# Kernel optimization log

Measured on AMD Instinct MI355X. Metric: run time of the kernel, lower is better.

The kernel has to match this reference:

```python
import math
import jax, jax.numpy as jnp
import numpy as np

EMBED_DIM = 1024
NUM_HEADS = 16
HEAD_DIM = EMBED_DIM // NUM_HEADS


def setup_inputs() -> dict:
    key = jax.random.key(0)
    ks = jax.random.split(key, 10)
    B, S, E = 2, 2048, EMBED_DIM
    x = jax.random.normal(ks[0], (B, S, E), dtype=jnp.float32)
    mask = jax.random.randint(ks[1], (B, S), 0, 2, dtype=jnp.int32)
    s = 1.0 / math.sqrt(E)
    Wq = jax.random.normal(ks[2], (E, E), dtype=jnp.float32) * s
    bq = jnp.zeros((E,), dtype=jnp.float32)
    Wk = jax.random.normal(ks[3], (E, E), dtype=jnp.float32) * s
    bk = jnp.zeros((E,), dtype=jnp.float32)
    Wv = jax.random.normal(ks[4], (E, E), dtype=jnp.float32) * s
    bv = jnp.zeros((E,), dtype=jnp.float32)
    Wo = jax.random.normal(ks[5], (E, E), dtype=jnp.float32) * s
    bo = jnp.zeros((E,), dtype=jnp.float32)
    return {"x": x, "mask": mask, "Wq": Wq, "bq": bq, "Wk": Wk, "bk": bk,
            "Wv": Wv, "bv": bv, "Wo": Wo, "bo": bo}


def reference(x, mask, Wq, bq, Wk, bk, Wv, bv, Wo, bo):
    B, S, E = x.shape
    H, D = NUM_HEADS, HEAD_DIM
    scale = math.sqrt(D)  # ScaledDotProductAttention built with head_dim

    def split_heads(t):
        return t.reshape(B, S, H, D).transpose(0, 2, 1, 3)  # [B,H,S,D]

    q = split_heads(x @ Wq + bq)
    k = split_heads(x @ Wk + bk)
    v = split_heads(x @ Wv + bv)

    scores = jnp.einsum('bhqd,bhkd->bhqk', q, k) / scale  # [B,H,S,S]
    m = mask[:, None, None, :].astype(scores.dtype)        # [B,1,1,S]
    neg = jnp.finfo(scores.dtype).min
    scores = jnp.where(m == 0, neg, scores)
    aw = jax.nn.softmax(scores, axis=-1)
    # post-softmax mask renormalization (as in the torch module)
    aw = aw * m
    denom = aw.sum(axis=-1, keepdims=True)
    aw = jnp.where(denom > 0, aw / jnp.where(denom > 0, denom, 1.0), 0.0)

    ctx = jnp.einsum('bhqk,bhkd->bhqd', aw, v)             # [B,H,S,D]
    ctx = ctx.transpose(0, 2, 1, 3).reshape(B, S, E)
    out = ctx @ Wo + bo
    return out
```

## Files before the change

### kernel.cpp

```cpp
#include <hip/hip_runtime.h>

typedef _Float16 half8 __attribute__((ext_vector_type(8)));
typedef _Float16 half4v __attribute__((ext_vector_type(4)));
typedef _Float16 h2 __attribute__((ext_vector_type(2)));
typedef float f4 __attribute__((ext_vector_type(4)));

#define ASYNC_COPY16(ldsp, gp)                                                     \
  __builtin_amdgcn_global_load_lds((__attribute__((address_space(1))) void*)(gp),  \
                                   (__attribute__((address_space(3))) void*)(ldsp),\
                                   16, 0, 0)

__device__ __forceinline__ f4 mfma16(half8 a, half8 b, f4 c) {
  return __builtin_amdgcn_mfma_f32_16x16x32_f16(a, b, c, 0, 0, 0);
}

__device__ __forceinline__ h2 pack2(float a, float b) {
  return __builtin_bit_cast(h2, __builtin_amdgcn_cvt_pkrtz(a, b));
}

#if defined(__has_builtin)
#if __has_builtin(__builtin_amdgcn_exp2f)
#define EXP2(x) __builtin_amdgcn_exp2f(x)
#endif
#endif
#ifndef EXP2
#define EXP2(x) __expf((x) * 0.69314718056f)
#endif
#define KSCALE 0.18033688011f
#define FIXMAX 10.0f


__global__ __launch_bounds__(256) void k_prep(
    const float* __restrict__ x, _Float16* __restrict__ xh,
    const float* __restrict__ Wq, const float* __restrict__ Wk,
    const float* __restrict__ Wv, const float* __restrict__ Wo,
    _Float16* __restrict__ wqkvT, _Float16* __restrict__ woT) {
  __shared__ float tw[32][33];
  const int bid = blockIdx.x, t = threadIdx.x;
  if (bid < 4096) {
    int i = (bid * 256 + t) * 4;
    f4 v = *(const f4*)(x + i);
    half4v h;
    h[0] = (_Float16)v[0]; h[1] = (_Float16)v[1];
    h[2] = (_Float16)v[2]; h[3] = (_Float16)v[3];
    *(half4v*)(xh + i) = h;
    return;
  }
  const int idx = bid - 4096;
  const int z = idx >> 10, rem = idx & 1023;
  const int n0 = (rem & 31) * 32, k0 = (rem >> 5) * 32;
  const float* w = (z == 0) ? Wq : (z == 1) ? Wk : (z == 2) ? Wv : Wo;
  _Float16* wt = (z == 3) ? woT : wqkvT + (size_t)z * 1048576;
  const int tx = t & 31, ty = t >> 5;
  for (int j = 0; j < 32; j += 8) tw[ty + j][tx] = w[(size_t)(k0 + ty + j) * 1024 + n0 + tx];
  __syncthreads();
  for (int j = 0; j < 32; j += 8)
    wt[(size_t)(n0 + ty + j) * 1024 + k0 + tx] = (_Float16)tw[tx][ty + j];
}

__global__ __launch_bounds__(256) void k_gemm_proj(
    const _Float16* __restrict__ A, const _Float16* __restrict__ Bt,
    const float* __restrict__ bq, const float* __restrict__ bk, const float* __restrict__ bv,
    _Float16* __restrict__ Qo, _Float16* __restrict__ Ko, _Float16* __restrict__ Vto) {
  __shared__ __align__(16) _Float16 As[128 * 32];
  __shared__ __align__(16) _Float16 Bs[128 * 32];
  const int t = threadIdx.x, lane = t & 63, w = t >> 6;
  const int qd = lane >> 4, lr = lane & 15;
  const int m0 = blockIdx.y * 128, n0 = blockIdx.x * 128;
  const int wm = (w & 1) * 64, wn = (w >> 1) * 64;
  const f4 z4 = {0.f, 0.f, 0.f, 0.f};
  f4 acc[4][4];
#pragma unroll
  for (int i = 0; i < 4; ++i)
#pragma unroll
    for (int j = 0; j < 4; ++j) acc[i][j] = z4;

  const int c0 = t, c1 = t + 256;
  for (int k0 = 0; k0 < 1024; k0 += 32) {
    const _Float16* ga0 = A + (size_t)(m0 + (c0 >> 2)) * 1024 + k0 + (c0 & 3) * 8;
    const _Float16* ga1 = A + (size_t)(m0 + (c1 >> 2)) * 1024 + k0 + (c1 & 3) * 8;
    const _Float16* gb0 = Bt + (size_t)(n0 + (c0 >> 2)) * 1024 + k0 + (c0 & 3) * 8;
    const _Float16* gb1 = Bt + (size_t)(n0 + (c1 >> 2)) * 1024 + k0 + (c1 & 3) * 8;
    char* la = (char*)As + w * 1024;
    char* lb = (char*)Bs + w * 1024;
    ASYNC_COPY16(la, ga0);
    ASYNC_COPY16(la + 4096, ga1);
    ASYNC_COPY16(lb, gb0);
    ASYNC_COPY16(lb + 4096, gb1);
    __syncthreads();
    half8 af[4], bf[4];
#pragma unroll
    for (int i = 0; i < 4; ++i)
      af[i] = *(const half8*)(As + (wm + i * 16 + lr) * 32 + qd * 8);
#pragma unroll
    for (int j = 0; j < 4; ++j)
      bf[j] = *(const half8*)(Bs + (wn + j * 16 + lr) * 32 + qd * 8);
#pragma unroll
    for (int i = 0; i < 4; ++i)
#pragma unroll
      for (int j = 0; j < 4; ++j) acc[i][j] = mfma16(af[i], bf[j], acc[i][j]);
    __syncthreads();
  }

  const int mat = n0 >> 10;
  const float* bias = (mat == 0) ? bq : (mat == 1) ? bk : bv;
  if (mat == 2) {
#pragma unroll
    for (int i = 0; i < 4; ++i)
#pragma unroll
      for (int j = 0; j < 4; ++j) {
        int n = (n0 + wn + j * 16 + lr) & 1023;
        int hh = n >> 6, d = n & 63;
        int mb = m0 + wm + i * 16 + qd * 4;
        int bb = mb >> 11, sb = mb & 2047;
        float bval = bias[n];
        half4v hv;
#pragma unroll
        for (int r = 0; r < 4; ++r) hv[r] = (_Float16)(acc[i][j][r] + bval);
        *(half4v*)(Vto + ((size_t)(bb * 16 + hh) * 64 + d) * 2048 + sb) = hv;
      }
  } else {
    _Float16* outp = (mat == 0) ? Qo : Ko;
    const float scl = (mat == 0) ? KSCALE : 1.f;
#pragma unroll
    for (int i = 0; i < 4; ++i)
#pragma unroll
      for (int j = 0; j < 4; ++j)
#pragma unroll
        for (int r = 0; r < 4; ++r) {
          int m = m0 + wm + i * 16 + qd * 4 + r;
          int n = (n0 + wn + j * 16 + lr) & 1023;
          float v = (acc[i][j][r] + bias[n]) * scl;
          int bb = m >> 11, s = m & 2047, hh = n >> 6, d = n & 63;
          outp[(size_t)((bb * 16 + hh) * 2048 + s) * 64 + d] = (_Float16)v;
        }
  }
}

__global__ __launch_bounds__(256, 2) void k_attn(
    const _Float16* __restrict__ Qg, const _Float16* __restrict__ Kg,
    const _Float16* __restrict__ Vtg, const int* __restrict__ maskg,
    _Float16* __restrict__ Op, float* __restrict__ ml) {
  __shared__ __align__(16) _Float16 Ks[64][72];
  __shared__ __align__(16) _Float16 Vts[64][72];
  __shared__ __align__(16) _Float16 Pq[4][16][72];
  __shared__ float Msk[64];

  const int bh = blockIdx.y;
  const int b = bh >> 4;
  const int q0 = blockIdx.x * 256;
  const int z = blockIdx.z;
  const int kb = z * 1024;
  const int t = threadIdx.x, lane = t & 63, w = t >> 6;
  const int qd = lane >> 4, lr = lane & 15;

  half8 qf[4][2];
#pragma unroll
  for (int rt = 0; rt < 4; ++rt)
#pragma unroll
    for (int ks = 0; ks < 2; ++ks)
      qf[rt][ks] = *(const half8*)(Qg + (size_t)(bh * 2048 + q0 + w * 64 + rt * 16 + lr) * 64 +
                                   ks * 32 + qd * 8);

  const f4 z4 = {0.f, 0.f, 0.f, 0.f};
  f4 O[4][4];
  f4 Ol[4];
#pragma unroll
  for (int rt = 0; rt < 4; ++rt) {
    Ol[rt] = z4;
#pragma unroll
    for (int dt = 0; dt < 4; ++dt) O[rt][dt] = z4;
  }
  half8 ones8;
#pragma unroll
  for (int j = 0; j < 8; ++j) ones8[j] = (_Float16)1.f;

  const int sr0 = t >> 3, scc = (t & 7) * 8;
  const int sr1 = sr0 + 32;
  const _Float16* Kbase = Kg + (size_t)bh * 2048 * 64 + (size_t)kb * 64;
  const _Float16* Vtbase = Vtg + (size_t)bh * 64 * 2048 + kb;

  f4 kr0 = *(const f4*)(Kbase + (size_t)sr0 * 64 + scc);
  f4 kr1 = *(const f4*)(Kbase + (size_t)sr1 * 64 + scc);
  f4 vr0 = *(const f4*)(Vtbase + (size_t)sr0 * 2048 + scc);
  f4 vr1 = *(const f4*)(Vtbase + (size_t)sr1 * 2048 + scc);
  float mval = 0.f;
  if (t < 64) mval = maskg[b * 2048 + kb + t] ? -FIXMAX : -30010.f;

  for (int it = 0; it < 16; ++it) {
    __syncthreads();
    *(f4*)&Ks[sr0][scc] = kr0;
    *(f4*)&Ks[sr1][scc] = kr1;
    *(f4*)&Vts[sr0][scc] = vr0;
    *(f4*)&Vts[sr1][scc] = vr1;
    if (t < 64) Msk[t] = mval;
    __syncthreads();

    if (it < 15) {
      int kk = (it + 1) * 64;
      kr0 = *(const f4*)(Kbase + (size_t)(kk + sr0) * 64 + scc);
      kr1 = *(const f4*)(Kbase + (size_t)(kk + sr1) * 64 + scc);
      vr0 = *(const f4*)(Vtbase + (size_t)sr0 * 2048 + kk + scc);
      vr1 = *(const f4*)(Vtbase + (size_t)sr1 * 2048 + kk + scc);
      if (t < 64) mval = maskg[b * 2048 + kb + kk + t] ? -FIXMAX : -30010.f;
    }

    half8 kf0[4], kf1[4];
#pragma unroll
    for (int kt = 0; kt < 4; ++kt) {
      kf0[kt] = *(const half8*)&Ks[kt * 16 + lr][qd * 8];
      kf1[kt] = *(const half8*)&Ks[kt * 16 + lr][32 + qd * 8];
    }

    half8 bp[4][2];
#pragma unroll
    for (int rtp = 0; rtp < 2; ++rtp) {
      const int r0 = rtp * 2, r1 = rtp * 2 + 1;
      f4 sc[2][4];
#pragma unroll
      for (int kt = 0; kt < 4; ++kt) {
        f4 mv = *(const f4*)&Msk[kt * 16 + qd * 4];
        sc[0][kt] = mv;
        sc[1][kt] = mv;
      }
      __builtin_amdgcn_s_setprio(1);
#pragma unroll
      for (int kt = 0; kt < 4; ++kt) {
        sc[0][kt] = mfma16(kf0[kt], qf[r0][0], sc[0][kt]);
        sc[0][kt] = mfma16(kf1[kt], qf[r0][1], sc[0][kt]);
        sc[1][kt] = mfma16(kf0[kt], qf[r1][0], sc[1][kt]);
        sc[1][kt] = mfma16(kf1[kt], qf[r1][1], sc[1][kt]);
      }
      __builtin_amdgcn_s_setprio(0);

#pragma unroll
      for (int rr = 0; rr < 2; ++rr) {
        const int rt = rtp * 2 + rr;
#pragma unroll
        for (int kt = 0; kt < 4; ++kt) {
          float p0 = EXP2(sc[rr][kt][0]);
          float p1 = EXP2(sc[rr][kt][1]);
          float p2 = EXP2(sc[rr][kt][2]);
          float p3 = EXP2(sc[rr][kt][3]);
          half4v hv;
          hv.lo = pack2(p0, p1);
          hv.hi = pack2(p2, p3);
          *(half4v*)&Pq[w][lr][kt * 16 + qd * 4] = hv;
        }
        bp[rt][0] = *(const half8*)&Pq[w][lr][qd * 8];
        bp[rt][1] = *(const half8*)&Pq[w][lr][32 + qd * 8];
      }
    }

    __builtin_amdgcn_s_setprio(1);
#pragma unroll
    for (int dt = 0; dt < 4; ++dt) {
      half8 va0 = *(const half8*)&Vts[dt * 16 + lr][qd * 8];
      half8 va1 = *(const half8*)&Vts[dt * 16 + lr][32 + qd * 8];
#pragma unroll
      for (int rt = 0; rt < 4; ++rt) {
        O[rt][dt] = mfma16(va0, bp[rt][0], O[rt][dt]);
        O[rt][dt] = mfma16(va1, bp[rt][1], O[rt][dt]);
      }
    }
#pragma unroll
    for (int rt = 0; rt < 4; ++rt) {
      Ol[rt] = mfma16(ones8, bp[rt][0], Ol[rt]);
      Ol[rt] = mfma16(ones8, bp[rt][1], Ol[rt]);
    }
    __builtin_amdgcn_s_setprio(0);
  }

#pragma unroll
  for (int rt = 0; rt < 4; ++rt) {
    int qrow = q0 + w * 64 + rt * 16 + lr;
    size_t rowi = (size_t)(z * 32 + bh) * 2048 + qrow;
    _Float16* op = Op + rowi * 64;
#pragma unroll
    for (int dt = 0; dt < 4; ++dt) {
      half4v hv;
#pragma unroll
      for (int r = 0; r < 4; ++r) hv[r] = (_Float16)O[rt][dt][r];
      *(half4v*)(op + dt * 16 + qd * 4) = hv;
    }
    if (qd == 0) ml[rowi] = Ol[rt][0];
  }
}

__global__ __launch_bounds__(256) void k_gemm_out(
    const _Float16* __restrict__ Op, const float* __restrict__ ml,
    const _Float16* __restrict__ Bt,
    const float* __restrict__ bo, float* __restrict__ out) {
  __shared__ __align__(16) _Float16 As[64 * 32];
  __shared__ __align__(16) _Float16 Bs[128 * 32];
  const int t = threadIdx.x, lane = t & 63, w = t >> 6;
  const int qd = lane >> 4, lr = lane & 15;
  const int m0 = blockIdx.y * 64, n0 = blockIdx.x * 128;
  const int wm = (w & 1) * 32, wn = (w >> 1) * 64;
  const f4 z4 = {0.f, 0.f, 0.f, 0.f};
  f4 acc[2][4];
#pragma unroll
  for (int i = 0; i < 2; ++i)
#pragma unroll
    for (int j = 0; j < 4; ++j) acc[i][j] = z4;

  const int ar = t >> 2, ac8 = (t & 3) * 8;
  const int m = m0 + ar;
  const int b = m >> 11, s = m & 2047;

  const int c0 = t, c1 = t + 256;
  for (int k0 = 0; k0 < 1024; k0 += 32) {
    const int h = k0 >> 6;
    const int d0 = (k0 & 63) + ac8;
    const size_t r1 = (size_t)(b * 16 + h) * 2048 + s;
    const size_t r2 = r1 + (size_t)32 * 2048;
    const float inv = 1.f / fmaxf(ml[r1] + ml[r2], 1e-20f);
    half8 o1 = *(const half8*)(Op + r1 * 64 + d0);
    half8 o2 = *(const half8*)(Op + r2 * 64 + d0);
    half8 ha;
#pragma unroll
    for (int j = 0; j < 8; ++j)
      ha[j] = (_Float16)(((float)o1[j] + (float)o2[j]) * inv);
    *(half8*)(As + ar * 32 + ac8) = ha;

    const _Float16* gb0 = Bt + (size_t)(n0 + (c0 >> 2)) * 1024 + k0 + (c0 & 3) * 8;
    const _Float16* gb1 = Bt + (size_t)(n0 + (c1 >> 2)) * 1024 + k0 + (c1 & 3) * 8;
    char* lb = (char*)Bs + w * 1024;
    ASYNC_COPY16(lb, gb0);
    ASYNC_COPY16(lb + 4096, gb1);
    __syncthreads();
    half8 af[2], bf[4];
#pragma unroll
    for (int i = 0; i < 2; ++i)
      af[i] = *(const half8*)(As + (wm + i * 16 + lr) * 32 + qd * 8);
#pragma unroll
    for (int j = 0; j < 4; ++j)
      bf[j] = *(const half8*)(Bs + (wn + j * 16 + lr) * 32 + qd * 8);
#pragma unroll
    for (int i = 0; i < 2; ++i)
#pragma unroll
      for (int j = 0; j < 4; ++j) acc[i][j] = mfma16(af[i], bf[j], acc[i][j]);
    __syncthreads();
  }
#pragma unroll
  for (int i = 0; i < 2; ++i)
#pragma unroll
    for (int j = 0; j < 4; ++j)
#pragma unroll
      for (int r = 0; r < 4; ++r) {
        int mm = m0 + wm + i * 16 + qd * 4 + r;
        int n = n0 + wn + j * 16 + lr;
        out[(size_t)mm * 1024 + n] = acc[i][j][r] + bo[n];
      }
}

extern "C" void kernel_launch(void* const* d_in, const int* in_sizes, int n_in,
                              void* d_out, int out_size, void* d_ws, size_t ws_size,
                              hipStream_t stream) {
  const float* x = (const float*)d_in[0];
  const int* mask = (const int*)d_in[1];
  const float* Wq = (const float*)d_in[2];
  const float* bq = (const float*)d_in[3];
  const float* Wk = (const float*)d_in[4];
  const float* bk = (const float*)d_in[5];
  const float* Wv = (const float*)d_in[6];
  const float* bv = (const float*)d_in[7];
  const float* Wo = (const float*)d_in[8];
  const float* bo = (const float*)d_in[9];
  float* out = (float*)d_out;
  char* ws = (char*)d_ws;
  const size_t MB = 1 << 20;

  _Float16* Oph   = (_Float16*)(ws + 0);
  _Float16* xh    = (_Float16*)(ws + 0);
  _Float16* wqkvT = (_Float16*)(ws + 8 * MB);
  _Float16* woT   = (_Float16*)(ws + 16 * MB);
  _Float16* Qh    = (_Float16*)(ws + 18 * MB);
  _Float16* Kh    = (_Float16*)(ws + 26 * MB);
  _Float16* Vth   = (_Float16*)(ws + 34 * MB);
  float*    mlw   = (float*)   (ws + 42 * MB);

  k_prep<<<dim3(8192), dim3(256), 0, stream>>>(x, xh, Wq, Wk, Wv, Wo, wqkvT, woT);
  k_gemm_proj<<<dim3(24, 32), dim3(256), 0, stream>>>(xh, wqkvT, bq, bk, bv, Qh, Kh, Vth);
  k_attn<<<dim3(8, 32, 2), dim3(256), 0, stream>>>(Qh, Kh, Vth, mask, Oph, mlw);
  k_gemm_out<<<dim3(8, 64), dim3(256), 0, stream>>>(Oph, mlw, woT, bo, out);
}
```

Before: 201.2 us.

## Keep softmax probabilities in registers via 16x16x16 MFMA; prefetch combine inputs

The attention kernel no longer writes the exponentiated P tile to shared memory and reads it back in the B-operand layout. It keeps each 16x16 P block in registers and feeds it straight to 16x16x16 f16 MFMAs, matching V reads to that layout. This removes LDS traffic and round-trip latency but doubles the PV MFMA instruction count, each doing half the K-depth. The output projection kernel now precomputes the per-head inverse normalizers once and software-prefetches the next split-K partial outputs across the loop's barrier.

```diff
diff --git a/kernel.cpp b/kernel.cpp
--- a/kernel.cpp
+++ b/kernel.cpp
@@ -12,6 +12,10 @@
 
 __device__ __forceinline__ f4 mfma16(half8 a, half8 b, f4 c) {
   return __builtin_amdgcn_mfma_f32_16x16x32_f16(a, b, c, 0, 0, 0);
+}
+
+__device__ __forceinline__ f4 mfma16x16(half4v a, half4v b, f4 c) {
+  return __builtin_amdgcn_mfma_f32_16x16x16f16(a, b, c, 0, 0, 0);
 }
 
 __device__ __forceinline__ h2 pack2(float a, float b) {
@@ -143,7 +147,6 @@
     _Float16* __restrict__ Op, float* __restrict__ ml) {
   __shared__ __align__(16) _Float16 Ks[64][72];
   __shared__ __align__(16) _Float16 Vts[64][72];
-  __shared__ __align__(16) _Float16 Pq[4][16][72];
   __shared__ float Msk[64];
 
   const int bh = blockIdx.y;
@@ -171,9 +174,9 @@
 #pragma unroll
     for (int dt = 0; dt < 4; ++dt) O[rt][dt] = z4;
   }
-  half8 ones8;
-#pragma unroll
-  for (int j = 0; j < 8; ++j) ones8[j] = (_Float16)1.f;
+  half4v ones4;
+#pragma unroll
+  for (int j = 0; j < 4; ++j) ones4[j] = (_Float16)1.f;
 
   const int sr0 = t >> 3, scc = (t & 7) * 8;
   const int sr1 = sr0 + 32;
@@ -212,7 +215,7 @@
       kf1[kt] = *(const half8*)&Ks[kt * 16 + lr][32 + qd * 8];
     }
 
-    half8 bp[4][2];
+    half4v pf[4][4];
 #pragma unroll
     for (int rtp = 0; rtp < 2; ++rtp) {
       const int r0 = rtp * 2, r1 = rtp * 2 + 1;
@@ -245,29 +248,29 @@
           half4v hv;
           hv.lo = pack2(p0, p1);
           hv.hi = pack2(p2, p3);
-          *(half4v*)&Pq[w][lr][kt * 16 + qd * 4] = hv;
+          pf[rt][kt] = hv;
         }
-        bp[rt][0] = *(const half8*)&Pq[w][lr][qd * 8];
-        bp[rt][1] = *(const half8*)&Pq[w][lr][32 + qd * 8];
       }
     }
 
     __builtin_amdgcn_s_setprio(1);
 #pragma unroll
     for (int dt = 0; dt < 4; ++dt) {
-      half8 va0 = *(const half8*)&Vts[dt * 16 + lr][qd * 8];
-      half8 va1 = *(const half8*)&Vts[dt * 16 + lr][32 + qd * 8];
-#pragma unroll
-      for (int rt = 0; rt < 4; ++rt) {
-        O[rt][dt] = mfma16(va0, bp[rt][0], O[rt][dt]);
-        O[rt][dt] = mfma16(va1, bp[rt][1], O[rt][dt]);
-      }
-    }
-#pragma unroll
-    for (int rt = 0; rt < 4; ++rt) {
-      Ol[rt] = mfma16(ones8, bp[rt][0], Ol[rt]);
-      Ol[rt] = mfma16(ones8, bp[rt][1], Ol[rt]);
-    }
+      half4v va[4];
+#pragma unroll
+      for (int kt = 0; kt < 4; ++kt)
+        va[kt] = *(const half4v*)&Vts[dt * 16 + lr][kt * 16 + qd * 4];
+#pragma unroll
+      for (int rt = 0; rt < 4; ++rt)
+#pragma unroll
+        for (int kt = 0; kt < 4; ++kt)
+          O[rt][dt] = mfma16x16(va[kt], pf[rt][kt], O[rt][dt]);
+    }
+#pragma unroll
+    for (int rt = 0; rt < 4; ++rt)
+#pragma unroll
+      for (int kt = 0; kt < 4; ++kt)
+        Ol[rt] = mfma16x16(ones4, pf[rt][kt], Ol[rt]);
     __builtin_amdgcn_s_setprio(0);
   }
 
@@ -308,15 +311,20 @@
   const int m = m0 + ar;
   const int b = m >> 11, s = m & 2047;
 
+  float invh[16];
+#pragma unroll
+  for (int h = 0; h < 16; ++h) {
+    size_t r1 = (size_t)(b * 16 + h) * 2048 + s;
+    invh[h] = 1.f / fmaxf(ml[r1] + ml[r1 + (size_t)32 * 2048], 1e-20f);
+  }
+
   const int c0 = t, c1 = t + 256;
+  size_t rr1 = (size_t)(b * 16 + 0) * 2048 + s;
+  half8 o1 = *(const half8*)(Op + rr1 * 64 + ac8);
+  half8 o2 = *(const half8*)(Op + (rr1 + (size_t)32 * 2048) * 64 + ac8);
+
   for (int k0 = 0; k0 < 1024; k0 += 32) {
-    const int h = k0 >> 6;
-    const int d0 = (k0 & 63) + ac8;
-    const size_t r1 = (size_t)(b * 16 + h) * 2048 + s;
-    const size_t r2 = r1 + (size_t)32 * 2048;
-    const float inv = 1.f / fmaxf(ml[r1] + ml[r2], 1e-20f);
-    half8 o1 = *(const half8*)(Op + r1 * 64 + d0);
-    half8 o2 = *(const half8*)(Op + r2 * 64 + d0);
+    const float inv = invh[k0 >> 6];
     half8 ha;
 #pragma unroll
     for (int j = 0; j < 8; ++j)
@@ -329,6 +337,15 @@
     ASYNC_COPY16(lb, gb0);
     ASYNC_COPY16(lb + 4096, gb1);
     __syncthreads();
+
+    if (k0 < 992) {
+      int k1 = k0 + 32;
+      int h1 = k1 >> 6, d1 = (k1 & 63) + ac8;
+      size_t r1n = (size_t)(b * 16 + h1) * 2048 + s;
+      o1 = *(const half8*)(Op + r1n * 64 + d1);
+      o2 = *(const half8*)(Op + (r1n + (size_t)32 * 2048) * 64 + d1);
+    }
+
     half8 af[2], bf[4];
 #pragma unroll
     for (int i = 0; i < 2; ++i)
```

Result: slower. 212.9 us (+5.8%).
